# Kernel tuning notes

Hardware: AMD Instinct MI355X
Metric: run time of the kernel (lower is better)

The kernel has to match this reference:

```python
import jax, jax.numpy as jnp
import numpy as np

N, D = 8192, 32
SIGMA = 4.0
DAMPING = 0.5
MAX_ITER = 10
SHIFT_TOL = 1e-4


def _sqdist(a, b):
    # squared euclidean distances, (Na, Nb)
    sq = jnp.sum(a * a, axis=1)[:, None] + jnp.sum(b * b, axis=1)[None, :] - 2.0 * (a @ b.T)
    return jnp.maximum(sq, 0.0)


def setup_inputs() -> dict:
    key = jax.random.key(0)
    x = jax.random.normal(key, (N, D), dtype=jnp.float32)
    sigma = jnp.asarray(SIGMA, dtype=jnp.float32)  # learned scalar nn.Parameter
    return {"x": x, "sigma": sigma}


def _find_centroids(x, sigma):
    gamma = 1.0 / (2.0 * sigma ** 2)

    def body(carry, _):
        centroids, done = carry
        sq = _sqdist(x, centroids)              # (N, N); cdist(x,c)**2
        w = jnp.exp(-sq * gamma)                # gaussian kernel weights
        new_c = (w @ x) / jnp.sum(w, axis=1, keepdims=True)
        shift = jnp.linalg.norm(new_c - centroids, axis=1)
        # torch breaks BEFORE the damping update when max shift < tol
        done_new = done | (jnp.max(shift) < SHIFT_TOL)
        centroids = jnp.where(done_new, centroids,
                              DAMPING * centroids + (1.0 - DAMPING) * new_c)
        return (centroids, done_new), None

    (centroids, _), _ = jax.lax.scan(jax.remat(body), (x, jnp.asarray(False)), None, length=MAX_ITER)
    return centroids


def _nms_keep(x, centroids, threshold):
    n = centroids.shape[0]
    sq_pc = _sqdist(x, centroids)
    closest = jnp.argmin(sq_pc, axis=1)                      # (N,)
    scores = jnp.zeros((n,), jnp.int32).at[closest].add(1)   # counts per centroid
    sq_cc = _sqdist(centroids, centroids)
    overlap = (sq_cc < threshold ** 2) & ~jnp.eye(n, dtype=bool)
    order = jnp.argsort(-scores)                             # descending by score

    def body(keep, idx):
        active = keep[idx]
        keep2 = jnp.where(active, keep & ~overlap[idx], keep)
        keep2 = keep2.at[idx].set(jnp.where(active, scores[idx] > 0, keep2[idx]))
        return keep2, None

    keep, _ = jax.lax.scan(body, jnp.ones((n,), bool), order)
    return keep


def reference(x, sigma):
    centroids = _find_centroids(x, sigma)
    # threshold = sigma.item() in torch -> constant w.r.t. autodiff
    keep = _nms_keep(x, centroids, jax.lax.stop_gradient(sigma))
    # assignment over kept centroids only (dropped centroids get -inf cost -> 0 prob)
    cost = -jnp.sqrt(_sqdist(x, centroids) + 1e-12)
    cost = jnp.where(keep[None, :], cost, -jnp.inf)
    assignment = jax.nn.softmax(cost, axis=1)  # alpha == 1 branch
    return centroids, assignment, keep
```

## Files before the change

### kernel.cpp

```cpp
#include <hip/hip_runtime.h>
#include <math.h>

#define NPTS 8192
#define DIM 32
#define MAX_ITER 10
#define TOL 1e-4f
#define DAMP 0.5f
#define LOG2E 1.4426950408889634f

#define OFF_MSP   0u
#define OFF_CCUR  17301504u
#define OFF_CNEW  17563648u
#define OFF_NX    17825792u
#define OFF_NC    17833984u
#define OFF_PV    17842176u
#define OFF_PJ    18366464u
#define OFF_RKP   18890752u
#define OFF_MSH   19152896u
#define OFF_SCO   19152912u
#define OFF_ORD   19161104u

__global__ __launch_bounds__(256) void k_init(const float* __restrict__ x,
                                              float* __restrict__ c0,
                                              float* __restrict__ nx,
                                              float* __restrict__ nc,
                                              int* __restrict__ scores,
                                              unsigned int* __restrict__ msh) {
    int p = blockIdx.x * blockDim.x + threadIdx.x;
    const float4* xr = (const float4*)(x + (size_t)p * DIM);
    float4* cr = (float4*)(c0 + (size_t)p * DIM);
    float s = 0.f;
#pragma unroll
    for (int q = 0; q < 8; ++q) {
        float4 v = xr[q];
        cr[q] = v;
        s += v.x * v.x + v.y * v.y + v.z * v.z + v.w * v.w;
    }
    nx[p] = s;
    nc[p] = s;
    scores[p] = 0;
    if (blockIdx.x == 0 && threadIdx.x < 16) msh[threadIdx.x] = 0u;
}

__global__ __launch_bounds__(256)
__attribute__((amdgpu_waves_per_eu(2, 4)))
void k_ms2(const float* __restrict__ x,
           const float* __restrict__ nx,
           const float* __restrict__ c,
           const float* __restrict__ nc,
           const float* __restrict__ sigma_p,
           float* __restrict__ P) {
    __shared__ float sc[128 * 32];
    __shared__ float sxx[128 * 32];
    __shared__ float snc[128];

    int t = threadIdx.x;
    int wv = __builtin_amdgcn_readfirstlane(t >> 6);
    int lane = t & 63;
    int it = (int)blockIdx.x >> 6, js = (int)blockIdx.x & 63;
    int i0 = it * 512 + wv * 128 + lane;
    int i1 = i0 + 64;
    int jb = js * 128;

    float sg = sigma_p[0];
    float ng2 = -LOG2E / (2.f * sg * sg);

    float xi0[DIM], xi1[DIM];
    {
        const float4* xr0 = (const float4*)(x + (size_t)i0 * DIM);
        const float4* xr1 = (const float4*)(x + (size_t)i1 * DIM);
#pragma unroll
        for (int q = 0; q < 8; ++q) {
            float4 a = xr0[q], b = xr1[q];
            xi0[4 * q] = a.x; xi0[4 * q + 1] = a.y; xi0[4 * q + 2] = a.z; xi0[4 * q + 3] = a.w;
            xi1[4 * q] = b.x; xi1[4 * q + 1] = b.y; xi1[4 * q + 2] = b.z; xi1[4 * q + 3] = b.w;
        }
    }
    float nx0 = nx[i0], nx1 = nx[i1];

    {
        const float4* srcc = (const float4*)(c + (size_t)jb * DIM);
        const float4* srcx = (const float4*)(x + (size_t)jb * DIM);
        float4* dstc = (float4*)sc;
        float4* dstx = (float4*)sxx;
        for (int k = t; k < 1024; k += 256) { dstc[k] = srcc[k]; dstx[k] = srcx[k]; }
        if (t < 128) snc[t] = nc[jb + t];
    }
    __syncthreads();

    float acc0[DIM], acc1[DIM];
#pragma unroll
    for (int d = 0; d < DIM; ++d) { acc0[d] = 0.f; acc1[d] = 0.f; }
    float ws0 = 0.f, ws1 = 0.f;

    for (int jj = 0; jj < 128; ++jj) {
        int rb = jj * 32;
        float w0, w1;
        {
            float a0 = 0.f, a1 = 0.f, a2 = 0.f, a3 = 0.f;
            float b0 = 0.f, b1 = 0.f, b2 = 0.f, b3 = 0.f;
#pragma unroll
            for (int q = 0; q < 8; ++q) {
                float4 cv = *(const float4*)(sc + rb + 4 * q);
                a0 = fmaf(xi0[4 * q + 0], cv.x, a0);
                a1 = fmaf(xi0[4 * q + 1], cv.y, a1);
                a2 = fmaf(xi0[4 * q + 2], cv.z, a2);
                a3 = fmaf(xi0[4 * q + 3], cv.w, a3);
                b0 = fmaf(xi1[4 * q + 0], cv.x, b0);
                b1 = fmaf(xi1[4 * q + 1], cv.y, b1);
                b2 = fmaf(xi1[4 * q + 2], cv.z, b2);
                b3 = fmaf(xi1[4 * q + 3], cv.w, b3);
            }
            float ncj = snc[jj];
            float sq0 = fmaxf(fmaf(-2.f, (a0 + a1) + (a2 + a3), nx0 + ncj), 0.f);
            float sq1 = fmaxf(fmaf(-2.f, (b0 + b1) + (b2 + b3), nx1 + ncj), 0.f);
            w0 = __builtin_amdgcn_exp2f(ng2 * sq0);
            w1 = __builtin_amdgcn_exp2f(ng2 * sq1);
        }
        ws0 += w0; ws1 += w1;
#pragma unroll
        for (int q = 0; q < 8; ++q) {
            float4 xv = *(const float4*)(sxx + rb + 4 * q);
            acc0[4 * q + 0] = fmaf(w0, xv.x, acc0[4 * q + 0]);
            acc0[4 * q + 1] = fmaf(w0, xv.y, acc0[4 * q + 1]);
            acc0[4 * q + 2] = fmaf(w0, xv.z, acc0[4 * q + 2]);
            acc0[4 * q + 3] = fmaf(w0, xv.w, acc0[4 * q + 3]);
            acc1[4 * q + 0] = fmaf(w1, xv.x, acc1[4 * q + 0]);
            acc1[4 * q + 1] = fmaf(w1, xv.y, acc1[4 * q + 1]);
            acc1[4 * q + 2] = fmaf(w1, xv.z, acc1[4 * q + 2]);
            acc1[4 * q + 3] = fmaf(w1, xv.w, acc1[4 * q + 3]);
        }
    }

    size_t base = ((size_t)js * 33) * NPTS + i0;
#pragma unroll
    for (int d = 0; d < DIM; ++d) {
        P[base + (size_t)d * NPTS] = acc0[d];
        P[base + (size_t)d * NPTS + 64] = acc1[d];
    }
    P[base + (size_t)32 * NPTS] = ws0;
    P[base + (size_t)32 * NPTS + 64] = ws1;
}

__global__ __launch_bounds__(256) void k_reduce(const float* __restrict__ P,
                                                const float* __restrict__ c_cur,
                                                float* __restrict__ c_new,
                                                unsigned int* __restrict__ maxshift) {
    __shared__ float red[256][33];
    int t = threadIdx.x;
    int pl = t & 63, qs = t >> 6;
    int i = blockIdx.x * 64 + pl;
    float tot[33];
#pragma unroll
    for (int d = 0; d < 33; ++d) tot[d] = 0.f;
    for (int js = qs * 16; js < qs * 16 + 16; ++js) {
        size_t base = ((size_t)js * 33) * NPTS + i;
#pragma unroll
        for (int d = 0; d < 33; ++d) tot[d] += P[base + (size_t)d * NPTS];
    }
#pragma unroll
    for (int d = 0; d < 33; ++d) red[t][d] = tot[d];
    __syncthreads();
    if (t < 64) {
        int ii = blockIdx.x * 64 + t;
        float tt[33];
#pragma unroll
        for (int d = 0; d < 33; ++d)
            tt[d] = (red[t][d] + red[t + 64][d]) + (red[t + 128][d] + red[t + 192][d]);
        float ws = tt[32];
        float inv = __builtin_amdgcn_rcpf(ws);
        inv = inv * (2.f - ws * inv);
        const float* co = c_cur + (size_t)ii * DIM;
        float sh2 = 0.f;
        float ncv[DIM];
#pragma unroll
        for (int d = 0; d < DIM; ++d) {
            float v = tt[d] * inv;
            ncv[d] = v;
            float df = v - co[d];
            sh2 = fmaf(df, df, sh2);
        }
        float4* dst = (float4*)(c_new + (size_t)ii * DIM);
#pragma unroll
        for (int q = 0; q < 8; ++q)
            dst[q] = make_float4(ncv[4 * q], ncv[4 * q + 1], ncv[4 * q + 2], ncv[4 * q + 3]);
        atomicMax(maxshift, __float_as_uint(__builtin_amdgcn_sqrtf(sh2)));
    }
}

__global__ __launch_bounds__(256) void k_update(float* __restrict__ c_cur,
                                                const float* __restrict__ c_new,
                                                float* __restrict__ nc,
                                                const unsigned int* __restrict__ maxshift) {
    if (__uint_as_float(*maxshift) < TOL) return;
    int i = blockIdx.x * 256 + threadIdx.x;
    float4* cc = (float4*)(c_cur + (size_t)i * DIM);
    const float4* cn = (const float4*)(c_new + (size_t)i * DIM);
    float s = 0.f;
#pragma unroll
    for (int q = 0; q < 8; ++q) {
        float4 a = cc[q], b = cn[q];
        float4 r = make_float4(DAMP * a.x + (1.f - DAMP) * b.x,
                               DAMP * a.y + (1.f - DAMP) * b.y,
                               DAMP * a.z + (1.f - DAMP) * b.z,
                               DAMP * a.w + (1.f - DAMP) * b.w);
        cc[q] = r;
        s += r.x * r.x + r.y * r.y + r.z * r.z + r.w * r.w;
    }
    nc[i] = s;
}

__global__ __launch_bounds__(256, 2) void k_scores2(const float* __restrict__ x,
                                                    const float* __restrict__ nx,
                                                    const float* __restrict__ c,
                                                    const float* __restrict__ nc,
                                                    float* __restrict__ pv,
                                                    int* __restrict__ pj) {
    __shared__ float sc[256 * 32];
    __shared__ float snc[256];
    int t = threadIdx.x;
    int wv = __builtin_amdgcn_readfirstlane(t >> 6);
    int lane = t & 63;
    int it = (int)blockIdx.x >> 5, js = (int)blockIdx.x & 31;
    int p0 = it * 512 + wv * 128 + lane;
    int p1 = p0 + 64;
    int jb = js * 256;

    float xi0[DIM], xi1[DIM];
    {
        const float4* xr0 = (const float4*)(x + (size_t)p0 * DIM);
        const float4* xr1 = (const float4*)(x + (size_t)p1 * DIM);
#pragma unroll
        for (int q = 0; q < 8; ++q) {
            float4 a = xr0[q], b = xr1[q];
            xi0[4 * q] = a.x; xi0[4 * q + 1] = a.y; xi0[4 * q + 2] = a.z; xi0[4 * q + 3] = a.w;
            xi1[4 * q] = b.x; xi1[4 * q + 1] = b.y; xi1[4 * q + 2] = b.z; xi1[4 * q + 3] = b.w;
        }
    }
    float nxp0 = nx[p0], nxp1 = nx[p1];

    {
        const float4* srcc = (const float4*)(c + (size_t)jb * DIM);
        float4* dstc = (float4*)sc;
        for (int k = t; k < 2048; k += 256) dstc[k] = srcc[k];
        snc[t] = nc[jb + t];
    }
    __syncthreads();

    float bv0 = INFINITY, bv1 = INFINITY;
    int bj0 = jb, bj1 = jb;
    for (int jj = 0; jj < 256; ++jj) {
        int rb = jj * 32;
        float a0 = 0.f, a1 = 0.f, a2 = 0.f, a3 = 0.f;
        float b0 = 0.f, b1 = 0.f, b2 = 0.f, b3 = 0.f;
#pragma unroll
        for (int q = 0; q < 8; ++q) {
            float4 cv = *(const float4*)(sc + rb + 4 * q);
            a0 = fmaf(xi0[4 * q + 0], cv.x, a0);
            a1 = fmaf(xi0[4 * q + 1], cv.y, a1);
            a2 = fmaf(xi0[4 * q + 2], cv.z, a2);
            a3 = fmaf(xi0[4 * q + 3], cv.w, a3);
            b0 = fmaf(xi1[4 * q + 0], cv.x, b0);
            b1 = fmaf(xi1[4 * q + 1], cv.y, b1);
            b2 = fmaf(xi1[4 * q + 2], cv.z, b2);
            b3 = fmaf(xi1[4 * q + 3], cv.w, b3);
        }
        float ncj = snc[jj];
        float sq0 = fmaxf(fmaf(-2.f, (a0 + a1) + (a2 + a3), nxp0 + ncj), 0.f);
        float sq1 = fmaxf(fmaf(-2.f, (b0 + b1) + (b2 + b3), nxp1 + ncj), 0.f);
        if (sq0 < bv0) { bv0 = sq0; bj0 = jb + jj; }
        if (sq1 < bv1) { bv1 = sq1; bj1 = jb + jj; }
    }
    pv[(size_t)js * NPTS + p0] = bv0;
    pj[(size_t)js * NPTS + p0] = bj0;
    pv[(size_t)js * NPTS + p1] = bv1;
    pj[(size_t)js * NPTS + p1] = bj1;
}

__global__ __launch_bounds__(256) void k_score_comb(const float* __restrict__ pv,
                                                    const int* __restrict__ pj,
                                                    int* __restrict__ scores) {
    int p = blockIdx.x * 256 + threadIdx.x;
    float bv = pv[p];
    int bj = pj[p];
    for (int js = 1; js < 32; ++js) {
        float v = pv[(size_t)js * NPTS + p];
        int j = pj[(size_t)js * NPTS + p];
        if (v < bv) { bv = v; bj = j; }
    }
    atomicAdd(&scores[bj], 1);
}

__global__ __launch_bounds__(256) void k_rank_part(const int* __restrict__ scores,
                                                   int* __restrict__ rkp) {
    int t = threadIdx.x;
    int wv = __builtin_amdgcn_readfirstlane(t >> 6);
    int lane = t & 63;
    int it = (int)blockIdx.x >> 5, js = (int)blockIdx.x & 31;
    int p = it * 256 + wv * 64 + lane;
    int sp = scores[p];
    int j0 = js * 256;
    int r = 0;
    for (int jj = 0; jj < 256; ++jj) {
        int sj = scores[j0 + jj];
        int j = j0 + jj;
        r += (sj > sp) || (sj == sp && j < p);
    }
    rkp[(size_t)js * NPTS + p] = r;
}

__global__ __launch_bounds__(256) void k_rank_comb(const int* __restrict__ rkp,
                                                   int* __restrict__ order) {
    int p = blockIdx.x * 256 + threadIdx.x;
    int r = 0;
    for (int js = 0; js < 32; ++js) r += rkp[(size_t)js * NPTS + p];
    order[r] = p;
}

__global__ __launch_bounds__(1024) void k_nms(const float* __restrict__ c,
                                              const int* __restrict__ order,
                                              const int* __restrict__ scores,
                                              const float* __restrict__ sigma_p,
                                              float* __restrict__ keep_out) {
    __shared__ int s_ord[NPTS];
    __shared__ unsigned char kp[NPTS];
    __shared__ int s_first[16];
    __shared__ int s_next;
    int t = threadIdx.x;
    for (int q = t; q < NPTS; q += 1024) { s_ord[q] = order[q]; kp[q] = 1; }
    __syncthreads();
    float sg = sigma_p[0];
    float thr2 = sg * sg;

    int k = 0;
    while (k < NPTS) {
        int cand = k + t;
        bool hit = (cand < NPTS) && (kp[s_ord[cand]] != 0);
        unsigned long long b = __ballot(hit);
        int wave = t >> 6;
        if ((t & 63) == 0)
            s_first[wave] = b ? (k + (wave << 6) + (__ffsll((unsigned long long)b) - 1))
                              : 0x7fffffff;
        __syncthreads();
        if (t == 0) {
            int mn = s_first[0];
            for (int w2 = 1; w2 < 16; ++w2) mn = min(mn, s_first[w2]);
            s_next = mn;
        }
        __syncthreads();
        int kf = s_next;
        if (kf == 0x7fffffff) { k += 1024; continue; }

        int idx = s_ord[kf];
        float ci[DIM];
        const float4* cr = (const float4*)(c + (size_t)idx * DIM);
#pragma unroll
        for (int q = 0; q < 8; ++q) {
            float4 v = cr[q];
            ci[4 * q] = v.x; ci[4 * q + 1] = v.y; ci[4 * q + 2] = v.z; ci[4 * q + 3] = v.w;
        }
#pragma unroll
        for (int m2 = 0; m2 < 8; ++m2) {
            int j = t + m2 * 1024;
            const float4* cj = (const float4*)(c + (size_t)j * DIM);
            float sq = 0.f;
#pragma unroll
            for (int q = 0; q < 8; ++q) {
                float4 v = cj[q];
                float e0 = v.x - ci[4 * q], e1 = v.y - ci[4 * q + 1];
                float e2 = v.z - ci[4 * q + 2], e3 = v.w - ci[4 * q + 3];
                sq += e0 * e0 + e1 * e1 + e2 * e2 + e3 * e3;
            }
            if (j != idx && sq < thr2) kp[j] = 0;
        }
        __syncthreads();
        if (t == 0) kp[idx] = (scores[idx] > 0) ? 1 : 0;
        __syncthreads();
        k = kf + 1;
    }
    __syncthreads();
    for (int q = t; q < NPTS; q += 1024) keep_out[q] = kp[q] ? 1.0f : 0.0f;
}

__global__ __launch_bounds__(256, 2) void k_apass1(const float* __restrict__ x,
                                                   const float* __restrict__ nx,
                                                   const float* __restrict__ c,
                                                   const float* __restrict__ nc,
                                                   const float* __restrict__ keepf,
                                                   float* __restrict__ ps) {
    __shared__ float sc[256 * 32];
    __shared__ float snc[256];
    __shared__ float skp[256];
    int t = threadIdx.x;
    int wv = __builtin_amdgcn_readfirstlane(t >> 6);
    int lane = t & 63;
    int it = (int)blockIdx.x >> 5, js = (int)blockIdx.x & 31;
    int p0 = it * 512 + wv * 128 + lane;
    int p1 = p0 + 64;
    int jb = js * 256;

    float xi0[DIM], xi1[DIM];
    {
        const float4* xr0 = (const float4*)(x + (size_t)p0 * DIM);
        const float4* xr1 = (const float4*)(x + (size_t)p1 * DIM);
#pragma unroll
        for (int q = 0; q < 8; ++q) {
            float4 a = xr0[q], b = xr1[q];
            xi0[4 * q] = a.x; xi0[4 * q + 1] = a.y; xi0[4 * q + 2] = a.z; xi0[4 * q + 3] = a.w;
            xi1[4 * q] = b.x; xi1[4 * q + 1] = b.y; xi1[4 * q + 2] = b.z; xi1[4 * q + 3] = b.w;
        }
    }
    float nxp0 = nx[p0], nxp1 = nx[p1];

    {
        const float4* srcc = (const float4*)(c + (size_t)jb * DIM);
        float4* dstc = (float4*)sc;
        for (int k = t; k < 2048; k += 256) dstc[k] = srcc[k];
        snc[t] = nc[jb + t];
        skp[t] = (keepf[jb + t] > 0.5f) ? 0.f : -1e38f;
    }
    __syncthreads();

    float S0 = 0.f, S1 = 0.f;
    for (int jj = 0; jj < 256; ++jj) {
        int rb = jj * 32;
        float a0 = 0.f, a1 = 0.f, a2 = 0.f, a3 = 0.f;
        float b0 = 0.f, b1 = 0.f, b2 = 0.f, b3 = 0.f;
#pragma unroll
        for (int q = 0; q < 8; ++q) {
            float4 cv = *(const float4*)(sc + rb + 4 * q);
            a0 = fmaf(xi0[4 * q + 0], cv.x, a0);
            a1 = fmaf(xi0[4 * q + 1], cv.y, a1);
            a2 = fmaf(xi0[4 * q + 2], cv.z, a2);
            a3 = fmaf(xi0[4 * q + 3], cv.w, a3);
            b0 = fmaf(xi1[4 * q + 0], cv.x, b0);
            b1 = fmaf(xi1[4 * q + 1], cv.y, b1);
            b2 = fmaf(xi1[4 * q + 2], cv.z, b2);
            b3 = fmaf(xi1[4 * q + 3], cv.w, b3);
        }
        float ncj = snc[jj];
        float kadd = skp[jj];
        float sq0 = fmaxf(fmaf(-2.f, (a0 + a1) + (a2 + a3), nxp0 + ncj), 0.f);
        float sq1 = fmaxf(fmaf(-2.f, (b0 + b1) + (b2 + b3), nxp1 + ncj), 0.f);
        float r0 = __builtin_amdgcn_sqrtf(sq0 + 1e-12f);
        float r1 = __builtin_amdgcn_sqrtf(sq1 + 1e-12f);
        S0 += __builtin_amdgcn_exp2f(fmaf(r0, -LOG2E, kadd));
        S1 += __builtin_amdgcn_exp2f(fmaf(r1, -LOG2E, kadd));
    }
    ps[(size_t)js * NPTS + p0] = S0;
    ps[(size_t)js * NPTS + p1] = S1;
}

__global__ __launch_bounds__(256)
__attribute__((amdgpu_waves_per_eu(3, 4)))
void k_apass2(const float* __restrict__ x,
              const float* __restrict__ c,
              const float* __restrict__ keepf,
              const float* __restrict__ ps,
              float* __restrict__ A) {
    __shared__ float sx[128 * 36];
    __shared__ float snx[128];
    __shared__ float sscale[128];
    __shared__ float spart[256];
    int t = threadIdx.x;
    int wv = __builtin_amdgcn_readfirstlane(t >> 6);
    int lane = t & 63;
    int pt = (int)blockIdx.x >> 4, jt = (int)blockIdx.x & 15;
    int p0 = pt * 128, j0 = jt * 512;

    {
        const float4* src = (const float4*)(x + (size_t)p0 * DIM) + t * 4;
        int row = t >> 1, colh = (t & 1) * 16;
        float4* dst = (float4*)(sx + row * 36 + colh);
        float s = 0.f;
#pragma unroll
        for (int q = 0; q < 4; ++q) {
            float4 v = src[q];
            dst[q] = v;
            s += v.x * v.x + v.y * v.y + v.z * v.z + v.w * v.w;
        }
        spart[t] = s;
    }
    __syncthreads();
    if (t < 128) {
        snx[t] = spart[2 * t] + spart[2 * t + 1];
        float SS = 0.f;
        for (int js = 0; js < 32; ++js) SS += ps[(size_t)js * NPTS + p0 + t];
        sscale[t] = 1.f / SS;
    }

    int ja = j0 + wv * 64 + lane;
    int jbx = ja + 256;
    float cj0[DIM], cj1[DIM];
    float nc0 = 0.f, nc1 = 0.f;
    {
        const float4* cra = (const float4*)(c + (size_t)ja * DIM);
        const float4* crb = (const float4*)(c + (size_t)jbx * DIM);
#pragma unroll
        for (int q = 0; q < 8; ++q) {
            float4 va = cra[q], vb = crb[q];
            cj0[4 * q] = va.x; cj0[4 * q + 1] = va.y; cj0[4 * q + 2] = va.z; cj0[4 * q + 3] = va.w;
            cj1[4 * q] = vb.x; cj1[4 * q + 1] = vb.y; cj1[4 * q + 2] = vb.z; cj1[4 * q + 3] = vb.w;
            nc0 += va.x * va.x + va.y * va.y + va.z * va.z + va.w * va.w;
            nc1 += vb.x * vb.x + vb.y * vb.y + vb.z * vb.z + vb.w * vb.w;
        }
    }
    float kadd0 = (keepf[ja] > 0.5f) ? 0.f : -1e38f;
    float kadd1 = (keepf[jbx] > 0.5f) ? 0.f : -1e38f;
    __syncthreads();

    for (int pp = 0; pp < 128; ++pp) {
        int rb = pp * 36;
        float d0 = 0.f, d1 = 0.f, d2 = 0.f, d3 = 0.f;
        float e0 = 0.f, e1 = 0.f, e2 = 0.f, e3 = 0.f;
#pragma unroll
        for (int q = 0; q < 8; ++q) {
            float4 v = *(const float4*)(sx + rb + 4 * q);
            d0 = fmaf(cj0[4 * q + 0], v.x, d0);
            d1 = fmaf(cj0[4 * q + 1], v.y, d1);
            d2 = fmaf(cj0[4 * q + 2], v.z, d2);
            d3 = fmaf(cj0[4 * q + 3], v.w, d3);
            e0 = fmaf(cj1[4 * q + 0], v.x, e0);
            e1 = fmaf(cj1[4 * q + 1], v.y, e1);
            e2 = fmaf(cj1[4 * q + 2], v.z, e2);
            e3 = fmaf(cj1[4 * q + 3], v.w, e3);
        }
        float nxp = snx[pp], scl = sscale[pp];
        float sqa = fmaxf(fmaf(-2.f, (d0 + d1) + (d2 + d3), nxp + nc0), 0.f);
        float sqb = fmaxf(fmaf(-2.f, (e0 + e1) + (e2 + e3), nxp + nc1), 0.f);
        float ra = __builtin_amdgcn_sqrtf(sqa + 1e-12f);
        float rbq = __builtin_amdgcn_sqrtf(sqb + 1e-12f);
        float ta = fmaf(ra, -LOG2E, kadd0);
        float tb = fmaf(rbq, -LOG2E, kadd1);
        float* rowp = A + (size_t)(p0 + pp) * NPTS;
        rowp[ja] = __builtin_amdgcn_exp2f(ta) * scl;
        rowp[jbx] = __builtin_amdgcn_exp2f(tb) * scl;
    }
}

extern "C" void kernel_launch(void* const* d_in, const int* in_sizes, int n_in,
                              void* d_out, int out_size, void* d_ws, size_t ws_size,
                              hipStream_t stream) {
    const float* x = (const float*)d_in[0];
    const float* sigma = (const float*)d_in[1];

    float* out = (float*)d_out;
    float* OUT_C = out;
    float* A = out + (size_t)NPTS * DIM;
    float* OUT_K = A + (size_t)NPTS * NPTS;

    float* msP = A + OFF_MSP;
    float* c_cur = A + OFF_CCUR;
    float* c_new = A + OFF_CNEW;
    float* nx = A + OFF_NX;
    float* nc = A + OFF_NC;
    float* pv = A + OFF_PV;
    int* pj = (int*)(A + OFF_PJ);
    int* rkp = (int*)(A + OFF_RKP);
    unsigned int* msh = (unsigned int*)(A + OFF_MSH);
    int* scores = (int*)(A + OFF_SCO);
    int* order = (int*)(A + OFF_ORD);
    float* ps = (float*)d_ws;

    k_init<<<NPTS / 256, 256, 0, stream>>>(x, c_cur, nx, nc, scores, msh);
    for (int itr = 0; itr < MAX_ITER; ++itr) {
        k_ms2<<<1024, 256, 0, stream>>>(x, nx, c_cur, nc, sigma, msP);
        k_reduce<<<NPTS / 64, 256, 0, stream>>>(msP, c_cur, c_new, msh + itr);
        k_update<<<NPTS / 256, 256, 0, stream>>>(c_cur, c_new, nc, msh + itr);
    }
    hipMemcpyAsync(OUT_C, c_cur, (size_t)NPTS * DIM * sizeof(float),
                   hipMemcpyDeviceToDevice, stream);

    k_scores2<<<512, 256, 0, stream>>>(x, nx, OUT_C, nc, pv, pj);
    k_score_comb<<<NPTS / 256, 256, 0, stream>>>(pv, pj, scores);
    k_rank_part<<<1024, 256, 0, stream>>>(scores, rkp);
    k_rank_comb<<<NPTS / 256, 256, 0, stream>>>(rkp, order);
    k_nms<<<1, 1024, 0, stream>>>(OUT_C, order, scores, sigma, OUT_K);

    k_apass1<<<512, 256, 0, stream>>>(x, nx, OUT_C, nc, OUT_K, ps);
    k_apass2<<<1024, 256, 0, stream>>>(x, OUT_C, OUT_K, ps, A);
}
```

Measured before the change: 1.992 ms.

## Interleave centroid, point and norm data and drop LDS staging in hot kernels

Centroids, the matching x rows, centroid norm and keep flag are packed into one padded row per point. Hot loops in the mean-shift, score, and assignment passes now read wave-uniform rows straight from global memory (scalar/constant cache path) instead of staging tiles in shared memory behind a barrier. A small extract kernel replaces the memcpy. This removes LDS traffic and barriers and may raise occupancy, but it relies on cache-hit scalar loads whose latency may be exposed in the inner loop.

```diff
diff --git a/kernel.cpp b/kernel.cpp
--- a/kernel.cpp
+++ b/kernel.cpp
@@ -7,53 +7,47 @@
 #define TOL 1e-4f
 #define DAMP 0.5f
 #define LOG2E 1.4426950408889634f
-
-#define OFF_MSP   0u
-#define OFF_CCUR  17301504u
-#define OFF_CNEW  17563648u
-#define OFF_NX    17825792u
-#define OFF_NC    17833984u
-#define OFF_PV    17842176u
-#define OFF_PJ    18366464u
-#define OFF_RKP   18890752u
-#define OFF_MSH   19152896u
-#define OFF_SCO   19152912u
-#define OFF_ORD   19161104u
+#define CXS 68
+
+#define OFF_MSP    0u
+#define OFF_CXF    17301504u
+#define OFF_CNEW   17858560u
+#define OFF_NX     18120704u
+#define OFF_PV     18128896u
+#define OFF_PJ     18391040u
+#define OFF_RKP    18653184u
+#define OFF_MSH    18915328u
+#define OFF_SCO    18915344u
+#define OFF_ORD    18923536u
 
 __global__ __launch_bounds__(256) void k_init(const float* __restrict__ x,
-                                              float* __restrict__ c0,
+                                              float* __restrict__ cxf,
                                               float* __restrict__ nx,
-                                              float* __restrict__ nc,
                                               int* __restrict__ scores,
                                               unsigned int* __restrict__ msh) {
     int p = blockIdx.x * blockDim.x + threadIdx.x;
     const float4* xr = (const float4*)(x + (size_t)p * DIM);
-    float4* cr = (float4*)(c0 + (size_t)p * DIM);
+    float* row = cxf + (size_t)p * CXS;
     float s = 0.f;
 #pragma unroll
     for (int q = 0; q < 8; ++q) {
         float4 v = xr[q];
-        cr[q] = v;
+        ((float4*)row)[q] = v;
+        ((float4*)row)[8 + q] = v;
         s += v.x * v.x + v.y * v.y + v.z * v.z + v.w * v.w;
     }
+    row[64] = s;
+    row[65] = 0.f;
     nx[p] = s;
-    nc[p] = s;
     scores[p] = 0;
     if (blockIdx.x == 0 && threadIdx.x < 16) msh[threadIdx.x] = 0u;
 }
 
-__global__ __launch_bounds__(256)
-__attribute__((amdgpu_waves_per_eu(2, 4)))
-void k_ms2(const float* __restrict__ x,
-           const float* __restrict__ nx,
-           const float* __restrict__ c,
-           const float* __restrict__ nc,
-           const float* __restrict__ sigma_p,
-           float* __restrict__ P) {
-    __shared__ float sc[128 * 32];
-    __shared__ float sxx[128 * 32];
-    __shared__ float snc[128];
-
+__global__ __launch_bounds__(256) void k_ms2(const float* __restrict__ x,
+                                             const float* __restrict__ nx,
+                                             const float* __restrict__ cxf,
+                                             const float* __restrict__ sigma_p,
+                                             float* __restrict__ P) {
     int t = threadIdx.x;
     int wv = __builtin_amdgcn_readfirstlane(t >> 6);
     int lane = t & 63;
@@ -78,30 +72,21 @@
     }
     float nx0 = nx[i0], nx1 = nx[i1];
 
-    {
-        const float4* srcc = (const float4*)(c + (size_t)jb * DIM);
-        const float4* srcx = (const float4*)(x + (size_t)jb * DIM);
-        float4* dstc = (float4*)sc;
-        float4* dstx = (float4*)sxx;
-        for (int k = t; k < 1024; k += 256) { dstc[k] = srcc[k]; dstx[k] = srcx[k]; }
-        if (t < 128) snc[t] = nc[jb + t];
-    }
-    __syncthreads();
-
     float acc0[DIM], acc1[DIM];
 #pragma unroll
     for (int d = 0; d < DIM; ++d) { acc0[d] = 0.f; acc1[d] = 0.f; }
     float ws0 = 0.f, ws1 = 0.f;
 
+    const float* row = cxf + (size_t)jb * CXS;
+
     for (int jj = 0; jj < 128; ++jj) {
-        int rb = jj * 32;
         float w0, w1;
         {
             float a0 = 0.f, a1 = 0.f, a2 = 0.f, a3 = 0.f;
             float b0 = 0.f, b1 = 0.f, b2 = 0.f, b3 = 0.f;
 #pragma unroll
             for (int q = 0; q < 8; ++q) {
-                float4 cv = *(const float4*)(sc + rb + 4 * q);
+                float4 cv = ((const float4*)row)[q];
                 a0 = fmaf(xi0[4 * q + 0], cv.x, a0);
                 a1 = fmaf(xi0[4 * q + 1], cv.y, a1);
                 a2 = fmaf(xi0[4 * q + 2], cv.z, a2);
@@ -111,7 +96,7 @@
                 b2 = fmaf(xi1[4 * q + 2], cv.z, b2);
                 b3 = fmaf(xi1[4 * q + 3], cv.w, b3);
             }
-            float ncj = snc[jj];
+            float ncj = row[64];
             float sq0 = fmaxf(fmaf(-2.f, (a0 + a1) + (a2 + a3), nx0 + ncj), 0.f);
             float sq1 = fmaxf(fmaf(-2.f, (b0 + b1) + (b2 + b3), nx1 + ncj), 0.f);
             w0 = __builtin_amdgcn_exp2f(ng2 * sq0);
@@ -120,7 +105,7 @@
         ws0 += w0; ws1 += w1;
 #pragma unroll
         for (int q = 0; q < 8; ++q) {
-            float4 xv = *(const float4*)(sxx + rb + 4 * q);
+            float4 xv = ((const float4*)row)[8 + q];
             acc0[4 * q + 0] = fmaf(w0, xv.x, acc0[4 * q + 0]);
             acc0[4 * q + 1] = fmaf(w0, xv.y, acc0[4 * q + 1]);
             acc0[4 * q + 2] = fmaf(w0, xv.z, acc0[4 * q + 2]);
@@ -130,6 +115,7 @@
             acc1[4 * q + 2] = fmaf(w1, xv.z, acc1[4 * q + 2]);
             acc1[4 * q + 3] = fmaf(w1, xv.w, acc1[4 * q + 3]);
         }
+        row += CXS;
     }
 
     size_t base = ((size_t)js * 33) * NPTS + i0;
@@ -143,7 +129,7 @@
 }
 
 __global__ __launch_bounds__(256) void k_reduce(const float* __restrict__ P,
-                                                const float* __restrict__ c_cur,
+                                                const float* __restrict__ cxf,
                                                 float* __restrict__ c_new,
                                                 unsigned int* __restrict__ maxshift) {
     __shared__ float red[256][33];
@@ -170,7 +156,7 @@
         float ws = tt[32];
         float inv = __builtin_amdgcn_rcpf(ws);
         inv = inv * (2.f - ws * inv);
-        const float* co = c_cur + (size_t)ii * DIM;
+        const float* co = cxf + (size_t)ii * CXS;
         float sh2 = 0.f;
         float ncv[DIM];
 #pragma unroll
@@ -188,36 +174,40 @@
     }
 }
 
-__global__ __launch_bounds__(256) void k_update(float* __restrict__ c_cur,
+__global__ __launch_bounds__(256) void k_update(float* __restrict__ cxf,
                                                 const float* __restrict__ c_new,
-                                                float* __restrict__ nc,
                                                 const unsigned int* __restrict__ maxshift) {
     if (__uint_as_float(*maxshift) < TOL) return;
     int i = blockIdx.x * 256 + threadIdx.x;
-    float4* cc = (float4*)(c_cur + (size_t)i * DIM);
+    float* row = cxf + (size_t)i * CXS;
     const float4* cn = (const float4*)(c_new + (size_t)i * DIM);
     float s = 0.f;
 #pragma unroll
     for (int q = 0; q < 8; ++q) {
-        float4 a = cc[q], b = cn[q];
+        float4 a = ((float4*)row)[q], b = cn[q];
         float4 r = make_float4(DAMP * a.x + (1.f - DAMP) * b.x,
                                DAMP * a.y + (1.f - DAMP) * b.y,
                                DAMP * a.z + (1.f - DAMP) * b.z,
                                DAMP * a.w + (1.f - DAMP) * b.w);
-        cc[q] = r;
+        ((float4*)row)[q] = r;
         s += r.x * r.x + r.y * r.y + r.z * r.z + r.w * r.w;
     }
-    nc[i] = s;
-}
-
-__global__ __launch_bounds__(256, 2) void k_scores2(const float* __restrict__ x,
-                                                    const float* __restrict__ nx,
-                                                    const float* __restrict__ c,
-                                                    const float* __restrict__ nc,
-                                                    float* __restrict__ pv,
-                                                    int* __restrict__ pj) {
-    __shared__ float sc[256 * 32];
-    __shared__ float snc[256];
+    row[64] = s;
+}
+
+__global__ __launch_bounds__(256) void k_extract(const float* __restrict__ cxf,
+                                                 float* __restrict__ outc) {
+    int g = blockIdx.x * 256 + threadIdx.x;
+    int rowi = g >> 3, q = g & 7;
+    ((float4*)(outc + (size_t)rowi * DIM))[q] =
+        ((const float4*)(cxf + (size_t)rowi * CXS))[q];
+}
+
+__global__ __launch_bounds__(256) void k_scores2(const float* __restrict__ x,
+                                                 const float* __restrict__ nx,
+                                                 const float* __restrict__ cxf,
+                                                 float* __restrict__ pv,
+                                                 int* __restrict__ pj) {
     int t = threadIdx.x;
     int wv = __builtin_amdgcn_readfirstlane(t >> 6);
     int lane = t & 63;
@@ -239,23 +229,15 @@
     }
     float nxp0 = nx[p0], nxp1 = nx[p1];
 
-    {
-        const float4* srcc = (const float4*)(c + (size_t)jb * DIM);
-        float4* dstc = (float4*)sc;
-        for (int k = t; k < 2048; k += 256) dstc[k] = srcc[k];
-        snc[t] = nc[jb + t];
-    }
-    __syncthreads();
-
+    const float* row = cxf + (size_t)jb * CXS;
     float bv0 = INFINITY, bv1 = INFINITY;
     int bj0 = jb, bj1 = jb;
     for (int jj = 0; jj < 256; ++jj) {
-        int rb = jj * 32;
         float a0 = 0.f, a1 = 0.f, a2 = 0.f, a3 = 0.f;
         float b0 = 0.f, b1 = 0.f, b2 = 0.f, b3 = 0.f;
 #pragma unroll
         for (int q = 0; q < 8; ++q) {
-            float4 cv = *(const float4*)(sc + rb + 4 * q);
+            float4 cv = ((const float4*)row)[q];
             a0 = fmaf(xi0[4 * q + 0], cv.x, a0);
             a1 = fmaf(xi0[4 * q + 1], cv.y, a1);
             a2 = fmaf(xi0[4 * q + 2], cv.z, a2);
@@ -265,11 +247,12 @@
             b2 = fmaf(xi1[4 * q + 2], cv.z, b2);
             b3 = fmaf(xi1[4 * q + 3], cv.w, b3);
         }
-        float ncj = snc[jj];
+        float ncj = row[64];
         float sq0 = fmaxf(fmaf(-2.f, (a0 + a1) + (a2 + a3), nxp0 + ncj), 0.f);
         float sq1 = fmaxf(fmaf(-2.f, (b0 + b1) + (b2 + b3), nxp1 + ncj), 0.f);
         if (sq0 < bv0) { bv0 = sq0; bj0 = jb + jj; }
         if (sq1 < bv1) { bv1 = sq1; bj1 = jb + jj; }
+        row += CXS;
     }
     pv[(size_t)js * NPTS + p0] = bv0;
     pj[(size_t)js * NPTS + p0] = bj0;
@@ -294,10 +277,8 @@
 __global__ __launch_bounds__(256) void k_rank_part(const int* __restrict__ scores,
                                                    int* __restrict__ rkp) {
     int t = threadIdx.x;
-    int wv = __builtin_amdgcn_readfirstlane(t >> 6);
-    int lane = t & 63;
     int it = (int)blockIdx.x >> 5, js = (int)blockIdx.x & 31;
-    int p = it * 256 + wv * 64 + lane;
+    int p = it * 256 + t;
     int sp = scores[p];
     int j0 = js * 256;
     int r = 0;
@@ -321,7 +302,8 @@
                                               const int* __restrict__ order,
                                               const int* __restrict__ scores,
                                               const float* __restrict__ sigma_p,
-                                              float* __restrict__ keep_out) {
+                                              float* __restrict__ keep_out,
+                                              float* __restrict__ cxf) {
     __shared__ int s_ord[NPTS];
     __shared__ unsigned char kp[NPTS];
     __shared__ int s_first[16];
@@ -379,18 +361,17 @@
         k = kf + 1;
     }
     __syncthreads();
-    for (int q = t; q < NPTS; q += 1024) keep_out[q] = kp[q] ? 1.0f : 0.0f;
-}
-
-__global__ __launch_bounds__(256, 2) void k_apass1(const float* __restrict__ x,
-                                                   const float* __restrict__ nx,
-                                                   const float* __restrict__ c,
-                                                   const float* __restrict__ nc,
-                                                   const float* __restrict__ keepf,
-                                                   float* __restrict__ ps) {
-    __shared__ float sc[256 * 32];
-    __shared__ float snc[256];
-    __shared__ float skp[256];
+    for (int q = t; q < NPTS; q += 1024) {
+        float kv = kp[q] ? 1.0f : 0.0f;
+        keep_out[q] = kv;
+        cxf[(size_t)q * CXS + 65] = kv;
+    }
+}
+
+__global__ __launch_bounds__(256) void k_apass1(const float* __restrict__ x,
+                                                const float* __restrict__ nx,
+                                                const float* __restrict__ cxf,
+                                                float* __restrict__ ps) {
     int t = threadIdx.x;
     int wv = __builtin_amdgcn_readfirstlane(t >> 6);
     int lane = t & 63;
@@ -412,23 +393,14 @@
     }
     float nxp0 = nx[p0], nxp1 = nx[p1];
 
-    {
-        const float4* srcc = (const float4*)(c + (size_t)jb * DIM);
-        float4* dstc = (float4*)sc;
-        for (int k = t; k < 2048; k += 256) dstc[k] = srcc[k];
-        snc[t] = nc[jb + t];
-        skp[t] = (keepf[jb + t] > 0.5f) ? 0.f : -1e38f;
-    }
-    __syncthreads();
-
+    const float* row = cxf + (size_t)jb * CXS;
     float S0 = 0.f, S1 = 0.f;
     for (int jj = 0; jj < 256; ++jj) {
-        int rb = jj * 32;
         float a0 = 0.f, a1 = 0.f, a2 = 0.f, a3 = 0.f;
         float b0 = 0.f, b1 = 0.f, b2 = 0.f, b3 = 0.f;
 #pragma unroll
         for (int q = 0; q < 8; ++q) {
-            float4 cv = *(const float4*)(sc + rb + 4 * q);
+            float4 cv = ((const float4*)row)[q];
             a0 = fmaf(xi0[4 * q + 0], cv.x, a0);
             a1 = fmaf(xi0[4 * q + 1], cv.y, a1);
             a2 = fmaf(xi0[4 * q + 2], cv.z, a2);
@@ -438,52 +410,42 @@
             b2 = fmaf(xi1[4 * q + 2], cv.z, b2);
             b3 = fmaf(xi1[4 * q + 3], cv.w, b3);
         }
-        float ncj = snc[jj];
-        float kadd = skp[jj];
+        float ncj = row[64];
+        float kadd = (row[65] > 0.5f) ? 0.f : -1e38f;
         float sq0 = fmaxf(fmaf(-2.f, (a0 + a1) + (a2 + a3), nxp0 + ncj), 0.f);
         float sq1 = fmaxf(fmaf(-2.f, (b0 + b1) + (b2 + b3), nxp1 + ncj), 0.f);
         float r0 = __builtin_amdgcn_sqrtf(sq0 + 1e-12f);
         float r1 = __builtin_amdgcn_sqrtf(sq1 + 1e-12f);
         S0 += __builtin_amdgcn_exp2f(fmaf(r0, -LOG2E, kadd));
         S1 += __builtin_amdgcn_exp2f(fmaf(r1, -LOG2E, kadd));
+        row += CXS;
     }
     ps[(size_t)js * NPTS + p0] = S0;
     ps[(size_t)js * NPTS + p1] = S1;
 }
 
-__global__ __launch_bounds__(256)
-__attribute__((amdgpu_waves_per_eu(3, 4)))
-void k_apass2(const float* __restrict__ x,
-              const float* __restrict__ c,
-              const float* __restrict__ keepf,
-              const float* __restrict__ ps,
-              float* __restrict__ A) {
-    __shared__ float sx[128 * 36];
+__global__ __launch_bounds__(256) void k_apass2(const float* __restrict__ x,
+                                                const float* __restrict__ c,
+                                                const float* __restrict__ keepf,
+                                                const float* __restrict__ ps,
+                                                float* __restrict__ A) {
     __shared__ float snx[128];
     __shared__ float sscale[128];
-    __shared__ float spart[256];
     int t = threadIdx.x;
     int wv = __builtin_amdgcn_readfirstlane(t >> 6);
     int lane = t & 63;
     int pt = (int)blockIdx.x >> 4, jt = (int)blockIdx.x & 15;
     int p0 = pt * 128, j0 = jt * 512;
 
-    {
-        const float4* src = (const float4*)(x + (size_t)p0 * DIM) + t * 4;
-        int row = t >> 1, colh = (t & 1) * 16;
-        float4* dst = (float4*)(sx + row * 36 + colh);
+    if (t < 128) {
+        const float4* xr = (const float4*)(x + (size_t)(p0 + t) * DIM);
         float s = 0.f;
 #pragma unroll
-        for (int q = 0; q < 4; ++q) {
-            float4 v = src[q];
-            dst[q] = v;
+        for (int q = 0; q < 8; ++q) {
+            float4 v = xr[q];
             s += v.x * v.x + v.y * v.y + v.z * v.z + v.w * v.w;
         }
-        spart[t] = s;
-    }
-    __syncthreads();
-    if (t < 128) {
-        snx[t] = spart[2 * t] + spart[2 * t + 1];
+        snx[t] = s;
         float SS = 0.f;
         for (int js = 0; js < 32; ++js) SS += ps[(size_t)js * NPTS + p0 + t];
         sscale[t] = 1.f / SS;
@@ -509,13 +471,13 @@
     float kadd1 = (keepf[jbx] > 0.5f) ? 0.f : -1e38f;
     __syncthreads();
 
+    const float* xrow = x + (size_t)p0 * DIM;
     for (int pp = 0; pp < 128; ++pp) {
-        int rb = pp * 36;
         float d0 = 0.f, d1 = 0.f, d2 = 0.f, d3 = 0.f;
         float e0 = 0.f, e1 = 0.f, e2 = 0.f, e3 = 0.f;
 #pragma unroll
         for (int q = 0; q < 8; ++q) {
-            float4 v = *(const float4*)(sx + rb + 4 * q);
+            float4 v = ((const float4*)xrow)[q];
             d0 = fmaf(cj0[4 * q + 0], v.x, d0);
             d1 = fmaf(cj0[4 * q + 1], v.y, d1);
             d2 = fmaf(cj0[4 * q + 2], v.z, d2);
@@ -529,12 +491,13 @@
         float sqa = fmaxf(fmaf(-2.f, (d0 + d1) + (d2 + d3), nxp + nc0), 0.f);
         float sqb = fmaxf(fmaf(-2.f, (e0 + e1) + (e2 + e3), nxp + nc1), 0.f);
         float ra = __builtin_amdgcn_sqrtf(sqa + 1e-12f);
-        float rbq = __builtin_amdgcn_sqrtf(sqb + 1e-12f);
+        float rb = __builtin_amdgcn_sqrtf(sqb + 1e-12f);
         float ta = fmaf(ra, -LOG2E, kadd0);
-        float tb = fmaf(rbq, -LOG2E, kadd1);
+        float tb = fmaf(rb, -LOG2E, kadd1);
         float* rowp = A + (size_t)(p0 + pp) * NPTS;
         rowp[ja] = __builtin_amdgcn_exp2f(ta) * scl;
         rowp[jbx] = __builtin_amdgcn_exp2f(tb) * scl;
+        xrow += DIM;
     }
 }
 
@@ -550,10 +513,9 @@
     float* OUT_K = A + (size_t)NPTS * NPTS;
 
     float* msP = A + OFF_MSP;
-    float* c_cur = A + OFF_CCUR;
+    float* cxf = A + OFF_CXF;
     float* c_new = A + OFF_CNEW;
     float* nx = A + OFF_NX;
-    float* nc = A + OFF_NC;
     float* pv = A + OFF_PV;
     int* pj = (int*)(A + OFF_PJ);
     int* rkp = (int*)(A + OFF_RKP);
@@ -562,21 +524,20 @@
     int* order = (int*)(A + OFF_ORD);
     float* ps = (float*)d_ws;
 
-    k_init<<<NPTS / 256, 256, 0, stream>>>(x, c_cur, nx, nc, scores, msh);
+    k_init<<<NPTS / 256, 256, 0, stream>>>(x, cxf, nx, scores, msh);
     for (int itr = 0; itr < MAX_ITER; ++itr) {
-        k_ms2<<<1024, 256, 0, stream>>>(x, nx, c_cur, nc, sigma, msP);
-        k_reduce<<<NPTS / 64, 256, 0, stream>>>(msP, c_cur, c_new, msh + itr);
-        k_update<<<NPTS / 256, 256, 0, stream>>>(c_cur, c_new, nc, msh + itr);
-    }
-    hipMemcpyAsync(OUT_C, c_cur, (size_t)NPTS * DIM * sizeof(float),
-                   hipMemcpyDeviceToDevice, stream);
-
-    k_scores2<<<512, 256, 0, stream>>>(x, nx, OUT_C, nc, pv, pj);
+        k_ms2<<<1024, 256, 0, stream>>>(x, nx, cxf, sigma, msP);
+        k_reduce<<<NPTS / 64, 256, 0, stream>>>(msP, cxf, c_new, msh + itr);
+        k_update<<<NPTS / 256, 256, 0, stream>>>(cxf, c_new, msh + itr);
+    }
+    k_extract<<<NPTS * 8 / 256, 256, 0, stream>>>(cxf, OUT_C);
+
+    k_scores2<<<512, 256, 0, stream>>>(x, nx, cxf, pv, pj);
     k_score_comb<<<NPTS / 256, 256, 0, stream>>>(pv, pj, scores);
     k_rank_part<<<1024, 256, 0, stream>>>(scores, rkp);
     k_rank_comb<<<NPTS / 256, 256, 0, stream>>>(rkp, order);
-    k_nms<<<1, 1024, 0, stream>>>(OUT_C, order, scores, sigma, OUT_K);
-
-    k_apass1<<<512, 256, 0, stream>>>(x, nx, OUT_C, nc, OUT_K, ps);
+    k_nms<<<1, 1024, 0, stream>>>(OUT_C, order, scores, sigma, OUT_K, cxf);
+
+    k_apass1<<<512, 256, 0, stream>>>(x, nx, cxf, ps);
     k_apass2<<<1024, 256, 0, stream>>>(x, OUT_C, OUT_K, ps, A);
 }
```

Result: slower. 2.535 ms (+27.3%).
